# Optimization experiments

Measured on AMD Instinct MI355X. Metric: run time of the kernel, lower is better.

## Reference

```python
import jax, jax.numpy as jnp
import numpy as np

N = 128          # preconditioner matrix dim = 8*8*2
L8 = 8           # lattice extent
KAPPA = 0.276
MAXITER = 20
NENT = N * (N + 1) // 2  # 8256 lower-triangular entries
_rows, _cols = np.tril_indices(N)

G = [jnp.array([[0, 1], [1, 0]], dtype=jnp.complex64),          # gamma_1 = sigma_x
     jnp.array([[0, -1j], [1j, 0]], dtype=jnp.complex64)]        # gamma_2 = sigma_y
I2 = jnp.eye(2, dtype=jnp.complex64)


def _D(x, U):
    # Wilson-Dirac: x (B,8,8,2) spinor field, U (B,2,8,8) complex links.
    out = x
    for mu in range(2):
        ax = mu + 1
        Um = U[:, mu]                                  # U_mu(n)
        Umb = jnp.roll(jnp.conj(Um), 1, axis=ax)       # U_mu^dag(n-mu)
        fwd = Um[..., None] * jnp.roll(x, -1, axis=ax)  # U(n) x(n+mu)
        bwd = Umb[..., None] * jnp.roll(x, 1, axis=ax)  # U^dag(n-mu) x(n-mu)
        out = out - KAPPA * (jnp.einsum('st,bxyt->bxys', I2 - G[mu], fwd)
                             + jnp.einsum('st,bxyt->bxys', I2 + G[mu], bwd))
    return out


def _Ddag(y, U):
    # Adjoint of _D: projectors swap on forward/backward hops.
    out = y
    for mu in range(2):
        ax = mu + 1
        Um = U[:, mu]
        Umb = jnp.roll(jnp.conj(Um), 1, axis=ax)
        fwd = Um[..., None] * jnp.roll(y, -1, axis=ax)
        bwd = Umb[..., None] * jnp.roll(y, 1, axis=ax)
        out = out - KAPPA * (jnp.einsum('st,bxyt->bxys', I2 + G[mu], fwd)
                             + jnp.einsum('st,bxyt->bxys', I2 - G[mu], bwd))
    return out


def setup_inputs() -> dict:
    key = jax.random.key(0)
    k1, k2, k3, k4 = jax.random.split(key, 4)
    B = 2048
    return {
        'net_out_re': jax.random.normal(k1, (B, NENT), jnp.float32),
        'net_out_im': jax.random.normal(k2, (B, NENT), jnp.float32),
        'theta': jax.random.normal(k3, (B, 2, L8, L8), jnp.float32),
        'b': jax.random.uniform(k4, (B, L8, L8, 2), jnp.float32),
    }


def reference(net_out_re, net_out_im, theta, b):
    net_out = (net_out_re + 1j * net_out_im).astype(jnp.complex64)  # (B, 8256)
    U = jnp.exp(1j * theta).astype(jnp.complex64)                   # (B, 2, 8, 8)
    bc = b.astype(jnp.complex64)                                    # (B, 8, 8, 2)
    B = bc.shape[0]

    # Dense lower-triangular factor (scatter of net_out, as in upper_tri_mat).
    Lmat = jnp.zeros((B, N, N), jnp.complex64).at[:, _rows, _cols].set(net_out)

    def M(x):  # preconditioner: L^H (L v)
        v = x.reshape(B, -1)
        w = jnp.einsum('bij,bj->bi', Lmat, v)
        u = jnp.einsum('bji,bj->bi', jnp.conj(Lmat), w)
        return u.reshape(x.shape)

    def A(x):  # DDOpt = D^dag D (Hermitian PSD)
        return _Ddag(_D(x, U), U)

    def dot(a, c):  # batched complex inner product
        return jnp.sum(jnp.conj(a) * c, axis=(1, 2, 3), keepdims=True)

    x0 = jnp.zeros_like(bc)
    r = bc - A(x0)
    z = M(r)
    p = z
    rz = dot(r, z)

    def step(carry, _):
        x, r, p, rz = carry
        Ap = A(p)
        alpha = rz / dot(p, Ap)
        x = x + alpha * p
        r = r - alpha * Ap
        z = M(r)
        rz2 = dot(r, z)
        p = z + (rz2 / rz) * p
        return (x, r, p, rz2), None

    (x, _, _, _), _ = jax.lax.scan(step, (x0, r, p, rz), None, length=MAXITER)

    res = A(x) - bc
    rn = jnp.linalg.norm(res.reshape(B, -1), axis=1)  # real per-batch norms
    return jnp.mean(rn).astype(jnp.float32)
```

## Files before the change

kernel.cpp:

```cpp
#include <hip/hip_runtime.h>
#include <math.h>

#define NV 128
#define NTRI 8256
#define NPAD 8320
#define KAP 0.276f
#define MAXIT 20
#define TPB 512

__device__ __forceinline__ float2 f2(float x, float y){ return make_float2(x, y); }
__device__ __forceinline__ float2 cadd(float2 a, float2 b){ return make_float2(a.x+b.x, a.y+b.y); }
__device__ __forceinline__ float2 csub(float2 a, float2 b){ return make_float2(a.x-b.x, a.y-b.y); }
__device__ __forceinline__ float2 cmul(float2 a, float2 b){ return make_float2(a.x*b.x - a.y*b.y, a.x*b.y + a.y*b.x); }
__device__ __forceinline__ float2 cmulc(float2 a, float2 b){
  return make_float2(a.x*b.x + a.y*b.y, a.x*b.y - a.y*b.x); }
__device__ __forceinline__ float2 cmac(float2 acc, float2 a, float2 b){
  acc.x = fmaf(a.x, b.x, fmaf(-a.y, b.y, acc.x));
  acc.y = fmaf(a.x, b.y, fmaf( a.y, b.x, acc.y));
  return acc; }
__device__ __forceinline__ float2 cmacc(float2 acc, float2 a, float2 b){
  acc.x = fmaf(a.x, b.x, fmaf( a.y, b.y, acc.x));
  acc.y = fmaf(a.x, b.y, fmaf(-a.y, b.x, acc.y));
  return acc; }
__device__ __forceinline__ float2 cdiv(float2 n, float2 d){
  float s = 1.0f / fmaf(d.x, d.x, d.y*d.y);
  return make_float2((n.x*d.x + n.y*d.y)*s, (n.y*d.x - n.x*d.y)*s); }

__device__ __forceinline__ int rowoff(int r){ return ((r*(r+1)) >> 1) + ((r+1) >> 1); }

template<int EF>
__device__ __forceinline__ void dirac(const float2* __restrict__ U,
                                      const float2* __restrict__ vin,
                                      float2* __restrict__ vout, int t)
{
  if (t < NV) {
    const int s = t & 1, site = t >> 1;
    const int yi = site & 7, xi = site >> 3;
    const int xp = (xi+1)&7, xm = (xi-1)&7, yp = (yi+1)&7, ym = (yi-1)&7;
    float2 acc;
    {
      const int bf = (xp<<4) + (yi<<1);
      float2 fs = vin[bf + s], fo = vin[bf + (s^1)];
      float2 cf = (EF > 0) ? cadd(fs, fo) : csub(fs, fo);
      acc = cmul(U[(xi<<3)+yi], cf);
      const int bb = (xm<<4) + (yi<<1);
      float2 bs = vin[bb + s], bo = vin[bb + (s^1)];
      float2 cb = (EF > 0) ? csub(bs, bo) : cadd(bs, bo);
      acc = cadd(acc, cmulc(U[(xm<<3)+yi], cb));
    }
    {
      const float tg = s ? 1.0f : -1.0f;
      const float gf = (float)EF * tg;
      const int bf = (xi<<4) + (yp<<1);
      float2 fs = vin[bf + s], fo = vin[bf + (s^1)];
      float2 cf = make_float2(fmaf(-gf, fo.y, fs.x), fmaf(gf, fo.x, fs.y));
      acc = cadd(acc, cmul(U[64 + (xi<<3)+yi], cf));
      const float gb = -gf;
      const int bb = (xi<<4) + (ym<<1);
      float2 bs = vin[bb + s], bo = vin[bb + (s^1)];
      float2 cb = make_float2(fmaf(-gb, bo.y, bs.x), fmaf(gb, bo.x, bs.y));
      acc = cadd(acc, cmulc(U[64 + (xi<<3)+ym], cb));
    }
    float2 v0 = vin[t];
    vout[t] = make_float2(fmaf(-KAP, acc.x, v0.x), fmaf(-KAP, acc.y, v0.y));
  }
  __syncthreads();
}

__device__ __forceinline__ void precond(const float2* __restrict__ Lc2,
                                        const float2* __restrict__ vin,
                                        float2* __restrict__ wvv,
                                        float2* __restrict__ vout,
                                        int w, int g, int c)
{
  {
    const int r = (w << 4) + g;
    const int bR = rowoff(r);
    float2 acc = f2(0.f, 0.f);
    const int kc = w << 1;
    for (int k = 0; k < kc; ++k) {
      const int j0 = (k << 3) + (c << 1);
      float4 Lp = *(const float4*)&Lc2[bR + j0];
      float4 vp = *(const float4*)&vin[j0];
      acc = cmac(acc, f2(Lp.x, Lp.y), f2(vp.x, vp.y));
      acc = cmac(acc, f2(Lp.z, Lp.w), f2(vp.z, vp.w));
    }
    #pragma unroll
    for (int pk = 0; pk < 2; ++pk) {
      const int j0 = ((kc + pk) << 3) + (c << 1);
      float4 Lp = *(const float4*)&Lc2[bR + j0];
      float4 vp = *(const float4*)&vin[j0];
      float2 La = (j0     <= r) ? f2(Lp.x, Lp.y) : f2(0.f, 0.f);
      float2 Lb = (j0 + 1 <= r) ? f2(Lp.z, Lp.w) : f2(0.f, 0.f);
      acc = cmac(acc, La, f2(vp.x, vp.y));
      acc = cmac(acc, Lb, f2(vp.z, vp.w));
    }
    acc.x += __shfl_xor(acc.x, 1); acc.y += __shfl_xor(acc.y, 1);
    acc.x += __shfl_xor(acc.x, 2); acc.y += __shfl_xor(acc.y, 2);
    if (c == 0) wvv[r] = acc;
  }
  __syncthreads();
  {
    const int j = (w << 4) + g;
    float2 acc = f2(0.f, 0.f);
    const int kc = (w << 1) + 2;
    #pragma unroll
    for (int pk = 0; pk < 2; ++pk) {
      const int i0 = ((2*w + pk) << 3) + (c << 1);
      float2 La = Lc2[rowoff(i0)     + j];
      float2 Lb = Lc2[rowoff(i0 + 1) + j];
      float4 wp = *(const float4*)&wvv[i0];
      if (i0     < j) La = f2(0.f, 0.f);
      if (i0 + 1 < j) Lb = f2(0.f, 0.f);
      acc = cmacc(acc, La, f2(wp.x, wp.y));
      acc = cmacc(acc, Lb, f2(wp.z, wp.w));
    }
    for (int k = kc; k < 16; ++k) {
      const int i0 = (k << 3) + (c << 1);
      float2 La = Lc2[rowoff(i0)     + j];
      float2 Lb = Lc2[rowoff(i0 + 1) + j];
      float4 wp = *(const float4*)&wvv[i0];
      acc = cmacc(acc, La, f2(wp.x, wp.y));
      acc = cmacc(acc, Lb, f2(wp.z, wp.w));
    }
    acc.x += __shfl_xor(acc.x, 1); acc.y += __shfl_xor(acc.y, 1);
    acc.x += __shfl_xor(acc.x, 2); acc.y += __shfl_xor(acc.y, 2);
    if (c == 0) vout[j] = acc;
  }
  __syncthreads();
}

__device__ __forceinline__ float2 block_dot(const float2* __restrict__ a, const float2* __restrict__ c,
                            float2* __restrict__ scal, int t, int slot)
{
  if (t < NV) {
    float2 v = cmacc(f2(0.f,0.f), a[t], c[t]);
    #pragma unroll
    for (int off = 32; off > 0; off >>= 1) {
      v.x += __shfl_down(v.x, off, 64);
      v.y += __shfl_down(v.y, off, 64);
    }
    if ((t & 63) == 0) scal[(slot<<1) + (t >> 6)] = v;
  }
  __syncthreads();
  return cadd(scal[slot<<1], scal[(slot<<1)+1]);
}

extern "C" __global__ void __launch_bounds__(TPB, 4)
cg_loss_kernel(const float* __restrict__ nre, const float* __restrict__ nim,
               const float* __restrict__ theta, const float* __restrict__ bin,
               float* __restrict__ out, float invB)
{
  __shared__ __align__(16) float2 Lc2[NPAD];
  __shared__ __align__(16) float2 Uc[128];
  __shared__ __align__(16) float2 bv[NV], xv[NV], rv[NV], pv[NV];
  __shared__ __align__(16) float2 zv[NV], Apv[NV], tv[NV], wv[NV];
  __shared__ float2 scal[8];

  const int t = threadIdx.x;
  const long long b = blockIdx.x;
  const int w = t >> 6, lane = t & 63, g = lane >> 2, c = lane & 3;

  {
    const float* nreb = nre + b * NTRI;
    const float* nimb = nim + b * NTRI;
    for (int p = t; p < NTRI; p += TPB) {
      float re = nreb[p], im = nimb[p];
      int r = (int)((sqrtf(8.f * (float)p + 1.f) - 1.f) * 0.5f + 1e-3f);
      int tr = (r * (r + 1)) >> 1;
      if (tr > p)               { tr -= r; --r; }
      else if (tr + r + 1 <= p) { tr += r + 1; ++r; }
      const int jj = p - tr;
      Lc2[tr + ((r + 1) >> 1) + jj] = make_float2(re, im);
    }
  }
  if (t < NV) {
    float th = theta[b * 128 + t];
    float sn, cs;
    sincosf(th, &sn, &cs);
    Uc[t] = make_float2(cs, sn);
    float bb = bin[b * 128 + t];
    bv[t] = make_float2(bb, 0.f);
    xv[t] = make_float2(0.f, 0.f);
    rv[t] = make_float2(bb, 0.f);
  }
  __syncthreads();

  precond(Lc2, rv, wv, zv, w, g, c);
  if (t < NV) pv[t] = zv[t];
  float2 rz = block_dot(rv, zv, scal, t, 0);

  #pragma unroll 1
  for (int it = 0; it < MAXIT; ++it) {
    dirac<-1>(Uc, pv, tv, t);
    dirac<+1>(Uc, tv, Apv, t);
    float2 pAp = block_dot(pv, Apv, scal, t, 1);
    if (t < NV) {
      float2 alpha = cdiv(rz, pAp);
      xv[t] = cmac(xv[t], alpha, pv[t]);
      rv[t] = csub(rv[t], cmul(alpha, Apv[t]));
    }
    __syncthreads();
    precond(Lc2, rv, wv, zv, w, g, c);
    float2 rz2 = block_dot(rv, zv, scal, t, 0);
    if (t < NV) {
      float2 beta = cdiv(rz2, rz);
      pv[t] = cmac(zv[t], beta, pv[t]);
    }
    rz = rz2;
    __syncthreads();
  }

  dirac<-1>(Uc, xv, tv, t);
  dirac<+1>(Uc, tv, Apv, t);
  if (t < NV) {
    float2 d = csub(Apv[t], bv[t]);
    float v = fmaf(d.x, d.x, d.y * d.y);
    #pragma unroll
    for (int off = 32; off > 0; off >>= 1) v += __shfl_down(v, off, 64);
    if ((t & 63) == 0) scal[4 + (t >> 6)].x = v;
  }
  __syncthreads();
  if (t == 0) {
    float rn = sqrtf(scal[4].x + scal[5].x);
    atomicAdd(out, rn * invB);
  }
}

extern "C" void kernel_launch(void* const* d_in, const int* in_sizes, int n_in,
                              void* d_out, int out_size, void* d_ws, size_t ws_size,
                              hipStream_t stream)
{
  const float* nre   = (const float*)d_in[0];
  const float* nim   = (const float*)d_in[1];
  const float* theta = (const float*)d_in[2];
  const float* bin   = (const float*)d_in[3];
  float* out = (float*)d_out;
  const int B = in_sizes[0] / NTRI;

  hipMemsetAsync(out, 0, sizeof(float), stream);
  cg_loss_kernel<<<B, TPB, 0, stream>>>(nre, nim, theta, bin, out, 1.0f / (float)B);
}
```

Measured before the change: 513.1 us.

## Load-balance triangular preconditioner matvecs by pairing short and long rows per wave

Changes the shared-memory layout of the lower-triangular factor to rows padded to multiples of 8 and zero-fills the padding. This lets whole 8-wide chunks be processed without masking. Each wave pairs row r with row 127-r so every wave does the same amount of work in both the L·v and L^H·w matvecs, removing the imbalance where later waves handled much longer rows. The cost is extra LDS (8704 entries instead of 8320), a zero-fill pass with an extra barrier, and more complex indexing and cross-half shuffles. It also leaves a dead leftover computation in the code.

```diff
diff --git a/kernel.cpp b/kernel.cpp
--- a/kernel.cpp
+++ b/kernel.cpp
@@ -3,7 +3,7 @@
 
 #define NV 128
 #define NTRI 8256
-#define NPAD 8320
+#define NPAD8 8704
 #define KAP 0.276f
 #define MAXIT 20
 #define TPB 512
@@ -26,7 +26,17 @@
   float s = 1.0f / fmaf(d.x, d.x, d.y*d.y);
   return make_float2((n.x*d.x + n.y*d.y)*s, (n.y*d.x - n.x*d.y)*s); }
 
-__device__ __forceinline__ int rowoff(int r){ return ((r*(r+1)) >> 1) + ((r+1) >> 1); }
+__device__ __forceinline__ int rowoff8(int r){
+  const int a = r >> 3;
+  return ((a + 1) * ((a << 2) + (r & 7))) << 3;
+}
+
+__device__ __forceinline__ float2 red8(float2 v){
+  v.x += __shfl_xor(v.x, 1);  v.y += __shfl_xor(v.y, 1);
+  v.x += __shfl_xor(v.x, 2);  v.y += __shfl_xor(v.y, 2);
+  v.x += __shfl_xor(v.x, 32); v.y += __shfl_xor(v.y, 32);
+  return v;
+}
 
 template<int EF>
 __device__ __forceinline__ void dirac(const float2* __restrict__ U,
@@ -71,61 +81,87 @@
                                         const float2* __restrict__ vin,
                                         float2* __restrict__ wvv,
                                         float2* __restrict__ vout,
-                                        int w, int g, int c)
-{
+                                        int w, int lane)
+{
+  const int c  = lane & 3;
+  const int g  = lane >> 2;
+  const int q  = g & 7;
+  const int h  = g >> 3;
+  const int c2 = c << 1;
+  const int rlo = (w << 3) + q;
+  const int rhi = 127 - rlo;
+  const int bLo = rowoff8(rlo);
+  const int bHi = rowoff8(rhi);
+
   {
-    const int r = (w << 4) + g;
-    const int bR = rowoff(r);
-    float2 acc = f2(0.f, 0.f);
-    const int kc = w << 1;
-    for (int k = 0; k < kc; ++k) {
-      const int j0 = (k << 3) + (c << 1);
-      float4 Lp = *(const float4*)&Lc2[bR + j0];
-      float4 vp = *(const float4*)&vin[j0];
-      acc = cmac(acc, f2(Lp.x, Lp.y), f2(vp.x, vp.y));
-      acc = cmac(acc, f2(Lp.z, Lp.w), f2(vp.z, vp.w));
-    }
-    #pragma unroll
-    for (int pk = 0; pk < 2; ++pk) {
-      const int j0 = ((kc + pk) << 3) + (c << 1);
-      float4 Lp = *(const float4*)&Lc2[bR + j0];
-      float4 vp = *(const float4*)&vin[j0];
-      float2 La = (j0     <= r) ? f2(Lp.x, Lp.y) : f2(0.f, 0.f);
-      float2 Lb = (j0 + 1 <= r) ? f2(Lp.z, Lp.w) : f2(0.f, 0.f);
-      acc = cmac(acc, La, f2(vp.x, vp.y));
-      acc = cmac(acc, Lb, f2(vp.z, vp.w));
-    }
-    acc.x += __shfl_xor(acc.x, 1); acc.y += __shfl_xor(acc.y, 1);
-    acc.x += __shfl_xor(acc.x, 2); acc.y += __shfl_xor(acc.y, 2);
-    if (c == 0) wvv[r] = acc;
-  }
-  __syncthreads();
+    float2 a0 = f2(0.f, 0.f), a1 = f2(0.f, 0.f);
+    #pragma unroll
+    for (int i = 0; i < 8; ++i) {
+      if (i <= w) {
+        const int k  = h ? (8 - w + i) : i;
+        const int jo = (k << 3) + c2;
+        const int base = h ? bHi : bLo;
+        const float4 Lp = *(const float4*)&Lc2[base + jo];
+        const float4 vp = *(const float4*)&vin[jo];
+        a0 = cmac(cmac(a0, f2(Lp.x,Lp.y), f2(vp.x,vp.y)), f2(Lp.z,Lp.w), f2(vp.z,vp.w));
+      } else {
+        const int k  = h ? (8 - w + i) : (i - w - 1);
+        const int jo = (k << 3) + c2;
+        const float4 Lp = *(const float4*)&Lc2[bHi + jo];
+        const float4 vp = *(const float4*)&vin[jo];
+        a1 = cmac(cmac(a1, f2(Lp.x,Lp.y), f2(vp.x,vp.y)), f2(Lp.z,Lp.w), f2(vp.z,vp.w));
+      }
+    }
+    if (!h) {
+      const int jo = ((7 - w) << 3) + c2;
+      const float4 Lp = *(const float4*)&Lc2[bHi + jo];
+      const float4 vp = *(const float4*)&vin[jo];
+      a1 = cmac(cmac(a1, f2(Lp.x,Lp.y), f2(vp.x,vp.y)), f2(Lp.z,Lp.w), f2(vp.z,vp.w));
+    }
+    float2 vLo = h ? f2(0.f, 0.f) : a0;
+    float2 vHi = h ? cadd(a0, a1) : a1;
+    vLo = red8(vLo);
+    vHi = red8(vHi);
+    if (c == 0) wvv[h ? rhi : rlo] = h ? vHi : vLo;
+  }
+  __syncthreads();
+
   {
-    const int j = (w << 4) + g;
-    float2 acc = f2(0.f, 0.f);
-    const int kc = (w << 1) + 2;
-    #pragma unroll
-    for (int pk = 0; pk < 2; ++pk) {
-      const int i0 = ((2*w + pk) << 3) + (c << 1);
-      float2 La = Lc2[rowoff(i0)     + j];
-      float2 Lb = Lc2[rowoff(i0 + 1) + j];
-      float4 wp = *(const float4*)&wvv[i0];
-      if (i0     < j) La = f2(0.f, 0.f);
-      if (i0 + 1 < j) Lb = f2(0.f, 0.f);
-      acc = cmacc(acc, La, f2(wp.x, wp.y));
-      acc = cmacc(acc, Lb, f2(wp.z, wp.w));
-    }
-    for (int k = kc; k < 16; ++k) {
-      const int i0 = (k << 3) + (c << 1);
-      float2 La = Lc2[rowoff(i0)     + j];
-      float2 Lb = Lc2[rowoff(i0 + 1) + j];
-      float4 wp = *(const float4*)&wvv[i0];
-      acc = cmacc(acc, La, f2(wp.x, wp.y));
-      acc = cmacc(acc, Lb, f2(wp.z, wp.w));
-    }
-    acc.x += __shfl_xor(acc.x, 1); acc.y += __shfl_xor(acc.y, 1);
-    acc.x += __shfl_xor(acc.x, 2); acc.y += __shfl_xor(acc.y, 2);
-    if (c == 0) vout[j] = acc;
+    float2 a0 = f2(0.f, 0.f), a1 = f2(0.f, 0.f);
+    #pragma unroll
+    for (int i = 0; i < 8; ++i) {
+      int k, j;
+      if (i <= w) {
+        k = h ? (8 + i) : (15 - w + i);
+        j = h ? rlo : rhi;
+      } else {
+        k = h ? (8 + i) : (i - 1);
+        j = rlo;
+      }
+      const int u    = (k + 1) << 3;
+      const int off0 = u * ((k << 2) + c2) + j;
+      const int i0   = (k << 3) + c2;
+      const float2 La = Lc2[off0];
+      const float2 Lb = Lc2[off0 + u];
+      const float4 wp = *(const float4*)&wvv[i0];
+      if (i <= w) a0 = cmacc(cmacc(a0, La, f2(wp.x,wp.y)), Lb, f2(wp.z,wp.w));
+      else        a1 = cmacc(cmacc(a1, La, f2(wp.x,wp.y)), Lb, f2(wp.z,wp.w));
+    }
+    if (!h) {
+      const int off0 = (28 + c2 << 6) / 8 * 8;
+      (void)off0;
+      const int u2   = 64;
+      const int o0   = u2 * (28 + c2) + rlo;
+      const float2 La = Lc2[o0];
+      const float2 Lb = Lc2[o0 + u2];
+      const float4 wp = *(const float4*)&wvv[56 + c2];
+      a1 = cmacc(cmacc(a1, La, f2(wp.x,wp.y)), Lb, f2(wp.z,wp.w));
+    }
+    float2 vJhi = h ? f2(0.f, 0.f) : a0;
+    float2 vJlo = h ? cadd(a0, a1) : a1;
+    vJhi = red8(vJhi);
+    vJlo = red8(vJlo);
+    if (c == 0) vout[h ? rlo : rhi] = h ? vJlo : vJhi;
   }
   __syncthreads();
 }
@@ -151,7 +187,7 @@
                const float* __restrict__ theta, const float* __restrict__ bin,
                float* __restrict__ out, float invB)
 {
-  __shared__ __align__(16) float2 Lc2[NPAD];
+  __shared__ __align__(16) float2 Lc2[NPAD8];
   __shared__ __align__(16) float2 Uc[128];
   __shared__ __align__(16) float2 bv[NV], xv[NV], rv[NV], pv[NV];
   __shared__ __align__(16) float2 zv[NV], Apv[NV], tv[NV], wv[NV];
@@ -159,7 +195,21 @@
 
   const int t = threadIdx.x;
   const long long b = blockIdx.x;
-  const int w = t >> 6, lane = t & 63, g = lane >> 2, c = lane & 3;
+  const int w = t >> 6, lane = t & 63;
+
+  #pragma unroll
+  for (int p = t; p < NPAD8; p += TPB) Lc2[p] = make_float2(0.f, 0.f);
+  if (t < NV) {
+    float th = theta[b * 128 + t];
+    float sn, cs;
+    sincosf(th, &sn, &cs);
+    Uc[t] = make_float2(cs, sn);
+    float bb = bin[b * 128 + t];
+    bv[t] = make_float2(bb, 0.f);
+    xv[t] = make_float2(0.f, 0.f);
+    rv[t] = make_float2(bb, 0.f);
+  }
+  __syncthreads();
 
   {
     const float* nreb = nre + b * NTRI;
@@ -170,23 +220,12 @@
       int tr = (r * (r + 1)) >> 1;
       if (tr > p)               { tr -= r; --r; }
       else if (tr + r + 1 <= p) { tr += r + 1; ++r; }
-      const int jj = p - tr;
-      Lc2[tr + ((r + 1) >> 1) + jj] = make_float2(re, im);
-    }
-  }
-  if (t < NV) {
-    float th = theta[b * 128 + t];
-    float sn, cs;
-    sincosf(th, &sn, &cs);
-    Uc[t] = make_float2(cs, sn);
-    float bb = bin[b * 128 + t];
-    bv[t] = make_float2(bb, 0.f);
-    xv[t] = make_float2(0.f, 0.f);
-    rv[t] = make_float2(bb, 0.f);
-  }
-  __syncthreads();
-
-  precond(Lc2, rv, wv, zv, w, g, c);
+      Lc2[rowoff8(r) + (p - tr)] = make_float2(re, im);
+    }
+  }
+  __syncthreads();
+
+  precond(Lc2, rv, wv, zv, w, lane);
   if (t < NV) pv[t] = zv[t];
   float2 rz = block_dot(rv, zv, scal, t, 0);
 
@@ -201,7 +240,7 @@
       rv[t] = csub(rv[t], cmul(alpha, Apv[t]));
     }
     __syncthreads();
-    precond(Lc2, rv, wv, zv, w, g, c);
+    precond(Lc2, rv, wv, zv, w, lane);
     float2 rz2 = block_dot(rv, zv, scal, t, 0);
     if (t < NV) {
       float2 beta = cdiv(rz2, rz);
```

Measured after the change: 522.1 us. No clear change (+1.8%).
